# Optimization experiments

Hardware: AMD Instinct MI355X
Metric: run time of the kernel (lower is better)

## Reference

```python
import jax, jax.numpy as jnp
import numpy as np

NEG_SLOPE = 0.2

def _gat(x_src, x_dst, W_src, W_dst, a_src, a_dst, bias, src, dst, num_dst):
    # Bipartite PyG GATConv, heads=1, concat, add_self_loops=False.
    h_src = x_src @ W_src              # [N_src, H]
    h_dst = x_dst @ W_dst              # [N_dst, H]
    # Per-edge attention logits: leaky_relu(a_src.h_src[i] + a_dst.h_dst[j])
    e = jax.nn.leaky_relu((h_src @ a_src)[src] + (h_dst @ a_dst)[dst], NEG_SLOPE)  # [E]
    # Segment softmax over incoming edges of each dst node
    m = jax.ops.segment_max(e, dst, num_segments=num_dst)
    m = jnp.where(jnp.isfinite(m), m, 0.0)  # empty segments -> safe
    ex = jnp.exp(e - m[dst])
    denom = jax.ops.segment_sum(ex, dst, num_segments=num_dst)
    alpha = ex / denom[dst]            # [E]
    # Scatter-sum weighted source messages
    out = jax.ops.segment_sum(alpha[:, None] * h_src[src], dst, num_segments=num_dst)
    return out + bias


def setup_inputs() -> dict:
    key = jax.random.key(0)
    ks = jax.random.split(key, 20)
    N_L, N_A, D, H, O, E = 100000, 20000, 128, 128, 64, 500000
    s = 1.0 / np.sqrt(D)
    inp = {
        'x_label': jax.random.normal(ks[0], (N_L, D), jnp.float32),
        'x_attr': jax.random.normal(ks[1], (N_A, D), jnp.float32),
        'W_src_la': jax.random.normal(ks[2], (D, H), jnp.float32) * s,
        'W_dst_la': jax.random.normal(ks[3], (D, H), jnp.float32) * s,
        'a_src_la': jax.random.normal(ks[4], (H,), jnp.float32) * s,
        'a_dst_la': jax.random.normal(ks[5], (H,), jnp.float32) * s,
        'b_la': jax.random.normal(ks[6], (H,), jnp.float32) * 0.01,
        'W_src_al': jax.random.normal(ks[7], (D, H), jnp.float32) * s,
        'W_dst_al': jax.random.normal(ks[8], (D, H), jnp.float32) * s,
        'a_src_al': jax.random.normal(ks[9], (H,), jnp.float32) * s,
        'a_dst_al': jax.random.normal(ks[10], (H,), jnp.float32) * s,
        'b_al': jax.random.normal(ks[11], (H,), jnp.float32) * 0.01,
        'W_lin': jax.random.normal(ks[12], (H, O), jnp.float32) * s,
        'b_lin': jax.random.normal(ks[13], (O,), jnp.float32) * 0.01,
        'edge_src_la': jax.random.randint(ks[14], (E,), 0, N_L, jnp.int32),
        'edge_dst_la': jax.random.randint(ks[15], (E,), 0, N_A, jnp.int32),
        'edge_src_al': jax.random.randint(ks[16], (E,), 0, N_A, jnp.int32),
        'edge_dst_al': jax.random.randint(ks[17], (E,), 0, N_L, jnp.int32),
    }
    return inp


def reference(x_label, x_attr, W_src_la, W_dst_la, a_src_la, a_dst_la, b_la,
              W_src_al, W_dst_al, a_src_al, a_dst_al, b_al, W_lin, b_lin,
              edge_src_la, edge_dst_la, edge_src_al, edge_dst_al):
    N_L = x_label.shape[0]
    N_A = x_attr.shape[0]
    # label -> attribute GAT (output for 'attribute' nodes)
    h_attr = _gat(x_label, x_attr, W_src_la, W_dst_la, a_src_la, a_dst_la, b_la,
                  edge_src_la, edge_dst_la, N_A)
    # attribute -> label GAT (output for 'label' nodes)
    h_label = _gat(x_attr, x_label, W_src_al, W_dst_al, a_src_al, a_dst_al, b_al,
                   edge_src_al, edge_dst_al, N_L)
    h_attr = jax.nn.relu(h_attr)  # computed as in original (unused downstream)
    h_label = jax.nn.relu(h_label)
    out = h_label @ W_lin + b_lin
    return out
```

## Files before the change

kernel.cpp:

```cpp
#include <hip/hip_runtime.h>
#include <math.h>

#define NEG_SLOPE 0.2f

typedef __attribute__((ext_vector_type(8))) short bf16x8;
typedef __attribute__((ext_vector_type(4))) float f32x4;

__device__ __forceinline__ unsigned short f2bf(float f) {
    unsigned u = __float_as_uint(f);
    unsigned r = (u + 0x7FFFu + ((u >> 16) & 1u)) >> 16;
    return (unsigned short)r;
}

__global__ void k_wdst(const float* __restrict__ Wd, const float* __restrict__ ad,
                       float* __restrict__ wdst) {
    int d = threadIdx.x;
    float s = 0.f;
    #pragma unroll 8
    for (int h = 0; h < 128; ++h) s += Wd[d * 128 + h] * ad[h];
    wdst[d] = s;
}

__global__ void k_rowdot(const float* __restrict__ X, const float* __restrict__ v,
                         float* __restrict__ out, int n) {
    int gw = (int)((blockIdx.x * blockDim.x + threadIdx.x) >> 6);
    int lane = threadIdx.x & 63;
    int half = lane >> 5, li = lane & 31;
    int row = gw * 2 + half;
    if (row >= n) return;
    const float4* X4 = (const float4*)X;
    const float4* V4 = (const float4*)v;
    float4 x = X4[(size_t)row * 32 + li];
    float4 b = V4[li];
    float p = x.x * b.x + x.y * b.y + x.z * b.z + x.w * b.w;
    #pragma unroll
    for (int off = 16; off; off >>= 1) p += __shfl_xor(p, off);
    if (li == 0) out[row] = p;
}

__global__ __launch_bounds__(256) void k_hsrc(const float* __restrict__ X,
                                              const float* __restrict__ W,
                                              float* __restrict__ H, int nrows) {
    __shared__ float Xs[32][128];
    int t = threadIdx.x;
    int row0 = blockIdx.x * 32;
    #pragma unroll
    for (int i = 0; i < 16; ++i) {
        int idx = t + i * 256;
        int r = idx >> 7;
        Xs[r][idx & 127] = (row0 + r < nrows) ? X[(size_t)row0 * 128 + idx] : 0.f;
    }
    __syncthreads();
    int cg = t & 31, rg = t >> 5;
    float acc[4][4];
    #pragma unroll
    for (int i = 0; i < 4; ++i)
        #pragma unroll
        for (int j = 0; j < 4; ++j) acc[i][j] = 0.f;
    const float4* W4 = (const float4*)W;
    #pragma unroll 4
    for (int d = 0; d < 128; ++d) {
        float4 wv = W4[d * 32 + cg];
        float x0 = Xs[rg * 4 + 0][d], x1 = Xs[rg * 4 + 1][d];
        float x2 = Xs[rg * 4 + 2][d], x3 = Xs[rg * 4 + 3][d];
        acc[0][0] += x0 * wv.x; acc[0][1] += x0 * wv.y; acc[0][2] += x0 * wv.z; acc[0][3] += x0 * wv.w;
        acc[1][0] += x1 * wv.x; acc[1][1] += x1 * wv.y; acc[1][2] += x1 * wv.z; acc[1][3] += x1 * wv.w;
        acc[2][0] += x2 * wv.x; acc[2][1] += x2 * wv.y; acc[2][2] += x2 * wv.z; acc[2][3] += x2 * wv.w;
        acc[3][0] += x3 * wv.x; acc[3][1] += x3 * wv.y; acc[3][2] += x3 * wv.z; acc[3][3] += x3 * wv.w;
    }
    #pragma unroll
    for (int i = 0; i < 4; ++i) {
        int gr = row0 + rg * 4 + i;
        if (gr < nrows) {
            float4 o = make_float4(acc[i][0], acc[i][1], acc[i][2], acc[i][3]);
            *(float4*)&H[(size_t)gr * 128 + cg * 4] = o;
        }
    }
}

__global__ void k_deg(const int* __restrict__ dst, int* __restrict__ deg, int E) {
    int i = blockIdx.x * blockDim.x + threadIdx.x;
    if (i < E) atomicAdd(&deg[dst[i]], 1);
}

__global__ __launch_bounds__(256) void k_scanA(const int* __restrict__ deg,
                                               int* __restrict__ bsum, int n) {
    __shared__ int sd[256];
    int t = threadIdx.x;
    int base = blockIdx.x * 1024 + t * 4;
    int s = 0;
    #pragma unroll
    for (int i = 0; i < 4; ++i) if (base + i < n) s += deg[base + i];
    sd[t] = s;
    __syncthreads();
    for (int off = 128; off; off >>= 1) {
        if (t < off) sd[t] += sd[t + off];
        __syncthreads();
    }
    if (t == 0) bsum[blockIdx.x] = sd[0];
}

__global__ __launch_bounds__(128) void k_scanB(int* __restrict__ bsum, int nb,
                                               int* __restrict__ rowptr, int n, int E) {
    __shared__ int ss[128];
    int t = threadIdx.x;
    if (nb <= 128) {
        int v = (t < nb) ? bsum[t] : 0;
        ss[t] = v;
        __syncthreads();
        for (int off = 1; off < 128; off <<= 1) {
            int u = (t >= off) ? ss[t - off] : 0;
            __syncthreads();
            ss[t] += u;
            __syncthreads();
        }
        if (t < nb) bsum[t] = ss[t] - v;
    } else if (t == 0) {
        int run = 0;
        for (int i = 0; i < nb; ++i) { int v = bsum[i]; bsum[i] = run; run += v; }
    }
    if (t == 0) rowptr[n] = E;
}

__global__ __launch_bounds__(256) void k_scanC(const int* __restrict__ deg,
                                               const int* __restrict__ bsum,
                                               int* __restrict__ rowptr, int n) {
    __shared__ int ss[256];
    int t = threadIdx.x;
    int base = blockIdx.x * 1024 + t * 4;
    int d[4]; int tsum = 0;
    #pragma unroll
    for (int i = 0; i < 4; ++i) { d[i] = (base + i < n) ? deg[base + i] : 0; tsum += d[i]; }
    ss[t] = tsum;
    __syncthreads();
    for (int off = 1; off < 256; off <<= 1) {
        int v = (t >= off) ? ss[t - off] : 0;
        __syncthreads();
        ss[t] += v;
        __syncthreads();
    }
    int excl = ss[t] - tsum + bsum[blockIdx.x];
    #pragma unroll
    for (int i = 0; i < 4; ++i) {
        if (base + i < n) rowptr[base + i] = excl;
        excl += d[i];
    }
}

__global__ void k_scatter(const int* __restrict__ src, const int* __restrict__ dst,
                          const float* __restrict__ ssrc, const float* __restrict__ sdst,
                          const int* __restrict__ rowptr, int* __restrict__ cursor,
                          int2* __restrict__ csr_pair, int E) {
    int i = blockIdx.x * blockDim.x + threadIdx.x;
    if (i >= E) return;
    int s = src[i], d = dst[i];
    float e = ssrc[s] + sdst[d];
    e = e > 0.f ? e : NEG_SLOPE * e;
    float ex = __expf(e);
    int pos = rowptr[d] + atomicAdd(&cursor[d], 1);
    csr_pair[pos] = make_int2(s, __float_as_int(ex));
}

__global__ __launch_bounds__(256) void k_gat(
    const int* __restrict__ rowptr, const int2* __restrict__ csr_pair,
    const float* __restrict__ H, const float* __restrict__ b_al,
    unsigned short* __restrict__ Gb, int n) {
    int t = threadIdx.x;
    int wave = t >> 6, lane = t & 63;
    int grp = lane >> 4, gl = lane & 15;
    int row = blockIdx.x * 16 + wave * 4 + grp;
    if (row >= n) return;
    int beg = rowptr[row], end = rowptr[row + 1];
    const float4* H4 = (const float4*)H;
    float4 aA = make_float4(0.f, 0.f, 0.f, 0.f);
    float4 aB = make_float4(0.f, 0.f, 0.f, 0.f);
    float denom = 0.f;
    int j = beg;
    for (; j + 4 <= end; j += 4) {
        int2 p0 = csr_pair[j], p1 = csr_pair[j + 1];
        int2 p2 = csr_pair[j + 2], p3 = csr_pair[j + 3];
        float x0 = __int_as_float(p0.y), x1 = __int_as_float(p1.y);
        float x2 = __int_as_float(p2.y), x3 = __int_as_float(p3.y);
        const float4* b0 = H4 + (size_t)p0.x * 32;
        const float4* b1 = H4 + (size_t)p1.x * 32;
        const float4* b2 = H4 + (size_t)p2.x * 32;
        const float4* b3 = H4 + (size_t)p3.x * 32;
        float4 h0a = b0[gl], h0b = b0[16 + gl];
        float4 h1a = b1[gl], h1b = b1[16 + gl];
        float4 h2a = b2[gl], h2b = b2[16 + gl];
        float4 h3a = b3[gl], h3b = b3[16 + gl];
        denom += (x0 + x1) + (x2 + x3);
        aA.x += x0 * h0a.x + x1 * h1a.x + x2 * h2a.x + x3 * h3a.x;
        aA.y += x0 * h0a.y + x1 * h1a.y + x2 * h2a.y + x3 * h3a.y;
        aA.z += x0 * h0a.z + x1 * h1a.z + x2 * h2a.z + x3 * h3a.z;
        aA.w += x0 * h0a.w + x1 * h1a.w + x2 * h2a.w + x3 * h3a.w;
        aB.x += x0 * h0b.x + x1 * h1b.x + x2 * h2b.x + x3 * h3b.x;
        aB.y += x0 * h0b.y + x1 * h1b.y + x2 * h2b.y + x3 * h3b.y;
        aB.z += x0 * h0b.z + x1 * h1b.z + x2 * h2b.z + x3 * h3b.z;
        aB.w += x0 * h0b.w + x1 * h1b.w + x2 * h2b.w + x3 * h3b.w;
    }
    for (; j + 2 <= end; j += 2) {
        int2 p0 = csr_pair[j], p1 = csr_pair[j + 1];
        float x0 = __int_as_float(p0.y), x1 = __int_as_float(p1.y);
        const float4* b0 = H4 + (size_t)p0.x * 32;
        const float4* b1 = H4 + (size_t)p1.x * 32;
        float4 h0a = b0[gl], h0b = b0[16 + gl];
        float4 h1a = b1[gl], h1b = b1[16 + gl];
        denom += x0 + x1;
        aA.x += x0 * h0a.x + x1 * h1a.x; aA.y += x0 * h0a.y + x1 * h1a.y;
        aA.z += x0 * h0a.z + x1 * h1a.z; aA.w += x0 * h0a.w + x1 * h1a.w;
        aB.x += x0 * h0b.x + x1 * h1b.x; aB.y += x0 * h0b.y + x1 * h1b.y;
        aB.z += x0 * h0b.z + x1 * h1b.z; aB.w += x0 * h0b.w + x1 * h1b.w;
    }
    if (j < end) {
        int2 p0 = csr_pair[j];
        float x0 = __int_as_float(p0.y);
        const float4* b0 = H4 + (size_t)p0.x * 32;
        float4 h0a = b0[gl], h0b = b0[16 + gl];
        denom += x0;
        aA.x += x0 * h0a.x; aA.y += x0 * h0a.y; aA.z += x0 * h0a.z; aA.w += x0 * h0a.w;
        aB.x += x0 * h0b.x; aB.y += x0 * h0b.y; aB.z += x0 * h0b.z; aB.w += x0 * h0b.w;
    }
    float inv = denom > 0.f ? 1.f / denom : 0.f;
    const float4* B4 = (const float4*)b_al;
    float4 bA = B4[gl], bB = B4[16 + gl];
    ushort4 ga, gb;
    ga.x = f2bf(fmaxf(aA.x * inv + bA.x, 0.f)); ga.y = f2bf(fmaxf(aA.y * inv + bA.y, 0.f));
    ga.z = f2bf(fmaxf(aA.z * inv + bA.z, 0.f)); ga.w = f2bf(fmaxf(aA.w * inv + bA.w, 0.f));
    gb.x = f2bf(fmaxf(aB.x * inv + bB.x, 0.f)); gb.y = f2bf(fmaxf(aB.y * inv + bB.y, 0.f));
    gb.z = f2bf(fmaxf(aB.z * inv + bB.z, 0.f)); gb.w = f2bf(fmaxf(aB.w * inv + bB.w, 0.f));
    unsigned short* Gr = Gb + (size_t)row * 128;
    *(ushort4*)(Gr + gl * 4) = ga;
    *(ushort4*)(Gr + 64 + gl * 4) = gb;
}

__global__ void k_wconv(const float* __restrict__ Wlin, unsigned short* __restrict__ Wb) {
    int idx = blockIdx.x * 256 + threadIdx.x;
    int col = idx >> 7, k = idx & 127;
    Wb[idx] = f2bf(Wlin[k * 64 + col]);
}

__global__ __launch_bounds__(256) void k_out_mfma(
    const unsigned short* __restrict__ Gb, const unsigned short* __restrict__ Wb,
    const float* __restrict__ b_lin, float* __restrict__ out, int n) {
    int t = threadIdx.x;
    int wave = t >> 6, lane = t & 63;
    int m = lane & 15, kq = lane >> 4;
    int row0 = blockIdx.x * 64 + wave * 16;
    int ra = row0 + m;
    if (ra >= n) ra = n - 1;
    const bf16x8* A = (const bf16x8*)(Gb + (size_t)ra * 128);
    f32x4 acc0 = {0.f, 0.f, 0.f, 0.f};
    f32x4 acc1 = {0.f, 0.f, 0.f, 0.f};
    f32x4 acc2 = {0.f, 0.f, 0.f, 0.f};
    f32x4 acc3 = {0.f, 0.f, 0.f, 0.f};
    const bf16x8* B0 = (const bf16x8*)(Wb + (size_t)(0 * 16 + m) * 128);
    const bf16x8* B1 = (const bf16x8*)(Wb + (size_t)(1 * 16 + m) * 128);
    const bf16x8* B2 = (const bf16x8*)(Wb + (size_t)(2 * 16 + m) * 128);
    const bf16x8* B3 = (const bf16x8*)(Wb + (size_t)(3 * 16 + m) * 128);
    #pragma unroll
    for (int s = 0; s < 4; ++s) {
        int ci = s * 4 + kq;
        bf16x8 a = A[ci];
        acc0 = __builtin_amdgcn_mfma_f32_16x16x32_bf16(a, B0[ci], acc0, 0, 0, 0);
        acc1 = __builtin_amdgcn_mfma_f32_16x16x32_bf16(a, B1[ci], acc1, 0, 0, 0);
        acc2 = __builtin_amdgcn_mfma_f32_16x16x32_bf16(a, B2[ci], acc2, 0, 0, 0);
        acc3 = __builtin_amdgcn_mfma_f32_16x16x32_bf16(a, B3[ci], acc3, 0, 0, 0);
    }
    float bl0 = b_lin[0 * 16 + m], bl1 = b_lin[1 * 16 + m];
    float bl2 = b_lin[2 * 16 + m], bl3 = b_lin[3 * 16 + m];
    #pragma unroll
    for (int j = 0; j < 4; ++j) {
        int row = row0 + kq * 4 + j;
        if (row < n) {
            float* orow = out + (size_t)row * 64;
            orow[0 * 16 + m] = acc0[j] + bl0;
            orow[1 * 16 + m] = acc1[j] + bl1;
            orow[2 * 16 + m] = acc2[j] + bl2;
            orow[3 * 16 + m] = acc3[j] + bl3;
        }
    }
}

extern "C" void kernel_launch(void* const* d_in, const int* in_sizes, int n_in,
                              void* d_out, int out_size, void* d_ws, size_t ws_size,
                              hipStream_t stream) {
    const float* x_label  = (const float*)d_in[0];
    const float* x_attr   = (const float*)d_in[1];
    const float* W_src_al = (const float*)d_in[7];
    const float* W_dst_al = (const float*)d_in[8];
    const float* a_src_al = (const float*)d_in[9];
    const float* a_dst_al = (const float*)d_in[10];
    const float* b_al     = (const float*)d_in[11];
    const float* W_lin    = (const float*)d_in[12];
    const float* b_lin    = (const float*)d_in[13];
    const int* edge_src   = (const int*)d_in[16];
    const int* edge_dst   = (const int*)d_in[17];

    const int D = 128;
    const int N_L = in_sizes[0] / D;
    const int N_A = in_sizes[1] / D;
    const int E   = in_sizes[16];
    const int nb  = (N_L + 1023) / 1024;

    float* ws = (float*)d_ws;
    float* h_src = ws;
    float* s_src = h_src + (size_t)N_A * 128;
    float* s_dst = s_src + N_A;
    float* wdst  = s_dst + N_L;
    int*   deg    = (int*)(wdst + 128);
    int*   cursor = deg + N_L;
    int*   rowptr = cursor + N_L;
    int*   bsum   = rowptr + N_L + 4;
    int2*  csr_pair = (int2*)(bsum + 128);
    unsigned short* Gb = (unsigned short*)(csr_pair + E);
    unsigned short* Wb = Gb + (size_t)(N_L + 64) * 128;
    float* out = (float*)d_out;

    hipMemsetAsync(deg, 0, (size_t)2 * N_L * sizeof(int), stream);

    k_wdst<<<1, 128, 0, stream>>>(W_dst_al, a_dst_al, wdst);
    k_rowdot<<<(N_L + 7) / 8, 256, 0, stream>>>(x_label, wdst, s_dst, N_L);
    k_hsrc<<<(N_A + 31) / 32, 256, 0, stream>>>(x_attr, W_src_al, h_src, N_A);
    k_rowdot<<<(N_A + 7) / 8, 256, 0, stream>>>(h_src, a_src_al, s_src, N_A);
    k_wconv<<<32, 256, 0, stream>>>(W_lin, Wb);
    k_deg<<<(E + 255) / 256, 256, 0, stream>>>(edge_dst, deg, E);
    k_scanA<<<nb, 256, 0, stream>>>(deg, bsum, N_L);
    k_scanB<<<1, 128, 0, stream>>>(bsum, nb, rowptr, N_L, E);
    k_scanC<<<nb, 256, 0, stream>>>(deg, bsum, rowptr, N_L);
    k_scatter<<<(E + 255) / 256, 256, 0, stream>>>(edge_src, edge_dst, s_src, s_dst,
                                                   rowptr, cursor, csr_pair, E);
    k_gat<<<(N_L + 15) / 16, 256, 0, stream>>>(rowptr, csr_pair, h_src, b_al, Gb, N_L);
    k_out_mfma<<<(N_L + 63) / 64, 256, 0, stream>>>(Gb, Wb, b_lin, out, N_L);
}
```

Before: 268.7 us.

## Store source projections as bf16 and compute source scores from folded weights

The source-node projection h_src is now written in bf16, which halves the bytes gathered per edge in the aggregation kernel, and each lane now loads one 16-byte chunk of 8 bf16 values. The source attention scores are computed from x_attr dotted with a folded W_src·a_src vector instead of reading back h_src. This makes the scores independent of the bf16 rounding. The cost is reduced precision in the aggregated messages, and the output column layout per lane changes to match.

Measured after the change: 258.5 us. -3.8%, faster.

```diff
diff --git a/kernel.cpp b/kernel.cpp
--- a/kernel.cpp
+++ b/kernel.cpp
@@ -12,13 +12,28 @@
     return (unsigned short)r;
 }
 
-__global__ void k_wdst(const float* __restrict__ Wd, const float* __restrict__ ad,
-                       float* __restrict__ wdst) {
-    int d = threadIdx.x;
+__device__ __forceinline__ void acc8(float* a, uint4 u, float x) {
+    a[0] += x * __uint_as_float(u.x << 16);
+    a[1] += x * __uint_as_float(u.x & 0xFFFF0000u);
+    a[2] += x * __uint_as_float(u.y << 16);
+    a[3] += x * __uint_as_float(u.y & 0xFFFF0000u);
+    a[4] += x * __uint_as_float(u.z << 16);
+    a[5] += x * __uint_as_float(u.z & 0xFFFF0000u);
+    a[6] += x * __uint_as_float(u.w << 16);
+    a[7] += x * __uint_as_float(u.w & 0xFFFF0000u);
+}
+
+__global__ void k_wvec(const float* __restrict__ Wd, const float* __restrict__ ad,
+                       const float* __restrict__ Ws, const float* __restrict__ as_,
+                       float* __restrict__ wdst, float* __restrict__ wsrc) {
+    int t = threadIdx.x;
+    const float* W = (t < 128) ? Wd : Ws;
+    const float* a = (t < 128) ? ad : as_;
+    int d = t & 127;
     float s = 0.f;
     #pragma unroll 8
-    for (int h = 0; h < 128; ++h) s += Wd[d * 128 + h] * ad[h];
-    wdst[d] = s;
+    for (int h = 0; h < 128; ++h) s += W[d * 128 + h] * a[h];
+    if (t < 128) wdst[d] = s; else wsrc[d] = s;
 }
 
 __global__ void k_rowdot(const float* __restrict__ X, const float* __restrict__ v,
@@ -40,7 +55,7 @@
 
 __global__ __launch_bounds__(256) void k_hsrc(const float* __restrict__ X,
                                               const float* __restrict__ W,
-                                              float* __restrict__ H, int nrows) {
+                                              unsigned short* __restrict__ Hb, int nrows) {
     __shared__ float Xs[32][128];
     int t = threadIdx.x;
     int row0 = blockIdx.x * 32;
@@ -72,8 +87,10 @@
     for (int i = 0; i < 4; ++i) {
         int gr = row0 + rg * 4 + i;
         if (gr < nrows) {
-            float4 o = make_float4(acc[i][0], acc[i][1], acc[i][2], acc[i][3]);
-            *(float4*)&H[(size_t)gr * 128 + cg * 4] = o;
+            ushort4 o;
+            o.x = f2bf(acc[i][0]); o.y = f2bf(acc[i][1]);
+            o.z = f2bf(acc[i][2]); o.w = f2bf(acc[i][3]);
+            *(ushort4*)&Hb[(size_t)gr * 128 + cg * 4] = o;
         }
     }
 }
@@ -163,7 +180,7 @@
 
 __global__ __launch_bounds__(256) void k_gat(
     const int* __restrict__ rowptr, const int2* __restrict__ csr_pair,
-    const float* __restrict__ H, const float* __restrict__ b_al,
+    const unsigned short* __restrict__ Hb, const float* __restrict__ b_al,
     unsigned short* __restrict__ Gb, int n) {
     int t = threadIdx.x;
     int wave = t >> 6, lane = t & 63;
@@ -171,9 +188,10 @@
     int row = blockIdx.x * 16 + wave * 4 + grp;
     if (row >= n) return;
     int beg = rowptr[row], end = rowptr[row + 1];
-    const float4* H4 = (const float4*)H;
-    float4 aA = make_float4(0.f, 0.f, 0.f, 0.f);
-    float4 aB = make_float4(0.f, 0.f, 0.f, 0.f);
+    const uint4* H16 = (const uint4*)Hb;
+    float a[8];
+    #pragma unroll
+    for (int k = 0; k < 8; ++k) a[k] = 0.f;
     float denom = 0.f;
     int j = beg;
     for (; j + 4 <= end; j += 4) {
@@ -181,57 +199,39 @@
         int2 p2 = csr_pair[j + 2], p3 = csr_pair[j + 3];
         float x0 = __int_as_float(p0.y), x1 = __int_as_float(p1.y);
         float x2 = __int_as_float(p2.y), x3 = __int_as_float(p3.y);
-        const float4* b0 = H4 + (size_t)p0.x * 32;
-        const float4* b1 = H4 + (size_t)p1.x * 32;
-        const float4* b2 = H4 + (size_t)p2.x * 32;
-        const float4* b3 = H4 + (size_t)p3.x * 32;
-        float4 h0a = b0[gl], h0b = b0[16 + gl];
-        float4 h1a = b1[gl], h1b = b1[16 + gl];
-        float4 h2a = b2[gl], h2b = b2[16 + gl];
-        float4 h3a = b3[gl], h3b = b3[16 + gl];
+        uint4 u0 = H16[(size_t)p0.x * 16 + gl];
+        uint4 u1 = H16[(size_t)p1.x * 16 + gl];
+        uint4 u2 = H16[(size_t)p2.x * 16 + gl];
+        uint4 u3 = H16[(size_t)p3.x * 16 + gl];
         denom += (x0 + x1) + (x2 + x3);
-        aA.x += x0 * h0a.x + x1 * h1a.x + x2 * h2a.x + x3 * h3a.x;
-        aA.y += x0 * h0a.y + x1 * h1a.y + x2 * h2a.y + x3 * h3a.y;
-        aA.z += x0 * h0a.z + x1 * h1a.z + x2 * h2a.z + x3 * h3a.z;
-        aA.w += x0 * h0a.w + x1 * h1a.w + x2 * h2a.w + x3 * h3a.w;
-        aB.x += x0 * h0b.x + x1 * h1b.x + x2 * h2b.x + x3 * h3b.x;
-        aB.y += x0 * h0b.y + x1 * h1b.y + x2 * h2b.y + x3 * h3b.y;
-        aB.z += x0 * h0b.z + x1 * h1b.z + x2 * h2b.z + x3 * h3b.z;
-        aB.w += x0 * h0b.w + x1 * h1b.w + x2 * h2b.w + x3 * h3b.w;
+        acc8(a, u0, x0); acc8(a, u1, x1); acc8(a, u2, x2); acc8(a, u3, x3);
     }
     for (; j + 2 <= end; j += 2) {
         int2 p0 = csr_pair[j], p1 = csr_pair[j + 1];
         float x0 = __int_as_float(p0.y), x1 = __int_as_float(p1.y);
-        const float4* b0 = H4 + (size_t)p0.x * 32;
-        const float4* b1 = H4 + (size_t)p1.x * 32;
-        float4 h0a = b0[gl], h0b = b0[16 + gl];
-        float4 h1a = b1[gl], h1b = b1[16 + gl];
+        uint4 u0 = H16[(size_t)p0.x * 16 + gl];
+        uint4 u1 = H16[(size_t)p1.x * 16 + gl];
         denom += x0 + x1;
-        aA.x += x0 * h0a.x + x1 * h1a.x; aA.y += x0 * h0a.y + x1 * h1a.y;
-        aA.z += x0 * h0a.z + x1 * h1a.z; aA.w += x0 * h0a.w + x1 * h1a.w;
-        aB.x += x0 * h0b.x + x1 * h1b.x; aB.y += x0 * h0b.y + x1 * h1b.y;
-        aB.z += x0 * h0b.z + x1 * h1b.z; aB.w += x0 * h0b.w + x1 * h1b.w;
+        acc8(a, u0, x0); acc8(a, u1, x1);
     }
     if (j < end) {
         int2 p0 = csr_pair[j];
         float x0 = __int_as_float(p0.y);
-        const float4* b0 = H4 + (size_t)p0.x * 32;
-        float4 h0a = b0[gl], h0b = b0[16 + gl];
+        uint4 u0 = H16[(size_t)p0.x * 16 + gl];
         denom += x0;
-        aA.x += x0 * h0a.x; aA.y += x0 * h0a.y; aA.z += x0 * h0a.z; aA.w += x0 * h0a.w;
-        aB.x += x0 * h0b.x; aB.y += x0 * h0b.y; aB.z += x0 * h0b.z; aB.w += x0 * h0b.w;
+        acc8(a, u0, x0);
     }
     float inv = denom > 0.f ? 1.f / denom : 0.f;
     const float4* B4 = (const float4*)b_al;
-    float4 bA = B4[gl], bB = B4[16 + gl];
+    float4 bA = B4[gl * 2], bB = B4[gl * 2 + 1];
     ushort4 ga, gb;
-    ga.x = f2bf(fmaxf(aA.x * inv + bA.x, 0.f)); ga.y = f2bf(fmaxf(aA.y * inv + bA.y, 0.f));
-    ga.z = f2bf(fmaxf(aA.z * inv + bA.z, 0.f)); ga.w = f2bf(fmaxf(aA.w * inv + bA.w, 0.f));
-    gb.x = f2bf(fmaxf(aB.x * inv + bB.x, 0.f)); gb.y = f2bf(fmaxf(aB.y * inv + bB.y, 0.f));
-    gb.z = f2bf(fmaxf(aB.z * inv + bB.z, 0.f)); gb.w = f2bf(fmaxf(aB.w * inv + bB.w, 0.f));
-    unsigned short* Gr = Gb + (size_t)row * 128;
-    *(ushort4*)(Gr + gl * 4) = ga;
-    *(ushort4*)(Gr + 64 + gl * 4) = gb;
+    ga.x = f2bf(fmaxf(a[0] * inv + bA.x, 0.f)); ga.y = f2bf(fmaxf(a[1] * inv + bA.y, 0.f));
+    ga.z = f2bf(fmaxf(a[2] * inv + bA.z, 0.f)); ga.w = f2bf(fmaxf(a[3] * inv + bA.w, 0.f));
+    gb.x = f2bf(fmaxf(a[4] * inv + bB.x, 0.f)); gb.y = f2bf(fmaxf(a[5] * inv + bB.y, 0.f));
+    gb.z = f2bf(fmaxf(a[6] * inv + bB.z, 0.f)); gb.w = f2bf(fmaxf(a[7] * inv + bB.w, 0.f));
+    unsigned short* Gr = Gb + (size_t)row * 128 + gl * 8;
+    *(ushort4*)Gr = ga;
+    *(ushort4*)(Gr + 4) = gb;
 }
 
 __global__ void k_wconv(const float* __restrict__ Wlin, unsigned short* __restrict__ Wb) {
@@ -304,32 +304,33 @@
     const int nb  = (N_L + 1023) / 1024;
 
     float* ws = (float*)d_ws;
-    float* h_src = ws;
-    float* s_src = h_src + (size_t)N_A * 128;
+    float* s_src = ws;
     float* s_dst = s_src + N_A;
     float* wdst  = s_dst + N_L;
-    int*   deg    = (int*)(wdst + 128);
+    float* wsrc  = wdst + 128;
+    int*   deg    = (int*)(wsrc + 128);
     int*   cursor = deg + N_L;
     int*   rowptr = cursor + N_L;
     int*   bsum   = rowptr + N_L + 4;
     int2*  csr_pair = (int2*)(bsum + 128);
-    unsigned short* Gb = (unsigned short*)(csr_pair + E);
+    unsigned short* Hb = (unsigned short*)(csr_pair + E);
+    unsigned short* Gb = Hb + (size_t)N_A * 128;
     unsigned short* Wb = Gb + (size_t)(N_L + 64) * 128;
     float* out = (float*)d_out;
 
     hipMemsetAsync(deg, 0, (size_t)2 * N_L * sizeof(int), stream);
 
-    k_wdst<<<1, 128, 0, stream>>>(W_dst_al, a_dst_al, wdst);
+    k_wvec<<<1, 256, 0, stream>>>(W_dst_al, a_dst_al, W_src_al, a_src_al, wdst, wsrc);
     k_rowdot<<<(N_L + 7) / 8, 256, 0, stream>>>(x_label, wdst, s_dst, N_L);
-    k_hsrc<<<(N_A + 31) / 32, 256, 0, stream>>>(x_attr, W_src_al, h_src, N_A);
-    k_rowdot<<<(N_A + 7) / 8, 256, 0, stream>>>(h_src, a_src_al, s_src, N_A);
+    k_rowdot<<<(N_A + 7) / 8, 256, 0, stream>>>(x_attr, wsrc, s_src, N_A);
     k_wconv<<<32, 256, 0, stream>>>(W_lin, Wb);
+    k_hsrc<<<(N_A + 31) / 32, 256, 0, stream>>>(x_attr, W_src_al, Hb, N_A);
     k_deg<<<(E + 255) / 256, 256, 0, stream>>>(edge_dst, deg, E);
     k_scanA<<<nb, 256, 0, stream>>>(deg, bsum, N_L);
     k_scanB<<<1, 128, 0, stream>>>(bsum, nb, rowptr, N_L, E);
     k_scanC<<<nb, 256, 0, stream>>>(deg, bsum, rowptr, N_L);
     k_scatter<<<(E + 255) / 256, 256, 0, stream>>>(edge_src, edge_dst, s_src, s_dst,
                                                    rowptr, cursor, csr_pair, E);
-    k_gat<<<(N_L + 15) / 16, 256, 0, stream>>>(rowptr, csr_pair, h_src, b_al, Gb, N_L);
+    k_gat<<<(N_L + 15) / 16, 256, 0, stream>>>(rowptr, csr_pair, Hb, b_al, Gb, N_L);
     k_out_mfma<<<(N_L + 63) / 64, 256, 0, stream>>>(Gb, Wb, b_lin, out, N_L);
 }
```
